# Performance work log

Measured on AMD Instinct MI355X. Metric: run time of the kernel, lower is better.

## Reference

```python
import jax, jax.numpy as jnp
import numpy as np

B, L, D = 4, 2048, 512   # batch, seq_len, model_dim
H, A = 8, 64             # head_num, atten_dim (H*A == D)
EPS = 1e-5


def setup_inputs() -> dict:
    key = jax.random.key(0)
    ks = jax.random.split(key, 20)
    std = 1.0 / np.sqrt(D)
    inp = {}
    for i, name in enumerate(["Q_data", "Q_time", "K_data", "K_time", "V_time"]):
        inp[name] = jax.random.normal(ks[i], (B, L, D), dtype=jnp.float32)
    # projection params (torch Linear: y = x @ W.T + b); store as [in, out]
    for i, name in enumerate(["Wq_d", "Wq_t", "Wk_d", "Wk_t", "Wv_t", "Wo"]):
        inp[name + "_w"] = jax.random.uniform(ks[5 + i], (D, H * A), jnp.float32, -std, std)
        inp[name + "_b"] = jax.random.uniform(ks[11 + i], (H * A,), jnp.float32, -std, std)
    inp["ln_g"] = jnp.ones((D,), jnp.float32)
    inp["ln_b"] = jnp.zeros((D,), jnp.float32)
    return inp


def _proj(x, w, b):
    # [B,L,D] -> [B,H,L,A]
    y = jnp.einsum('bld,de->ble', x, w) + b
    return y.reshape(B, L, H, A).transpose(0, 2, 1, 3)


def reference(Q_data, Q_time, K_data, K_time, V_time,
              Wq_d_w, Wq_t_w, Wk_d_w, Wk_t_w, Wv_t_w, Wo_w,
              Wq_d_b, Wq_t_b, Wk_d_b, Wk_t_b, Wv_t_b, Wo_b,
              ln_g, ln_b):
    residual = Q_data
    qd = _proj(Q_data, Wq_d_w, Wq_d_b)
    qt = _proj(Q_time, Wq_t_w, Wq_t_b)
    kd = _proj(K_data, Wk_d_w, Wk_d_b)
    kt = _proj(K_time, Wk_t_w, Wk_t_b)
    vt = _proj(V_time, Wv_t_w, Wv_t_b)
    scale = 1.0 / np.sqrt(A)
    # dual QK^T scores summed before softmax
    scores = (jnp.einsum('bhqa,bhka->bhqk', qd, kd)
              + jnp.einsum('bhqa,bhka->bhqk', qt, kt)) * scale
    attn = jax.nn.softmax(scores, axis=-1)
    ctx = jnp.einsum('bhqk,bhka->bhqa', attn, vt)        # [B,H,L,A]
    ctx = ctx.transpose(0, 2, 1, 3).reshape(B, L, H * A)  # [B,L,D]
    out = jnp.einsum('bld,de->ble', ctx, Wo_w) + Wo_b
    x = out + residual
    mu = jnp.mean(x, axis=-1, keepdims=True)
    var = jnp.var(x, axis=-1, keepdims=True)
    return (x - mu) / jnp.sqrt(var + EPS) * ln_g + ln_b
```

## Files before the change

kernel.cpp:

```cpp
#include <hip/hip_runtime.h>
#include <hip/hip_bf16.h>
#include <stdint.h>


using f32x4  = __attribute__((ext_vector_type(4))) float;
using bf16x8 = __attribute__((ext_vector_type(8))) short;

typedef __attribute__((address_space(1))) const uint32_t g_u32;
typedef __attribute__((address_space(3))) uint32_t l_u32;

#if __has_builtin(__builtin_amdgcn_exp2f)
#define EXP2F __builtin_amdgcn_exp2f
#else
#define EXP2F exp2f
#endif
#define QSCALE 0.1803368801111204f

__device__ __forceinline__ void glds16(const void* g, void* l) {
  __builtin_amdgcn_global_load_lds((g_u32*)g, (l_u32*)l, 16, 0, 0);
}

__device__ __forceinline__ unsigned short f2bfu(float f) {
  __hip_bfloat16 h = __float2bfloat16(f);
  union { __hip_bfloat16 h; unsigned short u; } v;
  v.h = h;
  return v.u;
}

__device__ __forceinline__ uint32_t pack_trunc(float lo, float hi) {
  union { float f; uint32_t u; } a, b;
  a.f = lo; b.f = hi;
  return __builtin_amdgcn_perm(b.u, a.u, 0x07060302u);
}

__global__ __launch_bounds__(256) void k_prep_w(
    const float* __restrict__ w0, const float* __restrict__ w1,
    const float* __restrict__ w2, const float* __restrict__ w3,
    const float* __restrict__ w4, const float* __restrict__ w5,
    unsigned short* __restrict__ wt) {
  __shared__ float tile[64][68];
  const float* wsrc[6] = {w0, w1, w2, w3, w4, w5};
  int bid = blockIdx.x;
  int mat = bid >> 6, tid = bid & 63;
  int k0 = (tid >> 3) << 6, c0 = (tid & 7) << 6;
  const float* w = wsrc[mat];
  int t = threadIdx.x;
  {
    int r = t >> 2, cq = (t & 3) << 4;
    const float4* src = reinterpret_cast<const float4*>(w + (size_t)(k0 + r) * 512 + c0 + cq);
#pragma unroll
    for (int j = 0; j < 4; ++j) {
      float4 v = src[j];
      tile[r][cq + j * 4 + 0] = v.x;
      tile[r][cq + j * 4 + 1] = v.y;
      tile[r][cq + j * 4 + 2] = v.z;
      tile[r][cq + j * 4 + 3] = v.w;
    }
  }
  __syncthreads();
  {
    int cc = t >> 2, kq = (t & 3) << 4;
    union { unsigned short u[16]; uint4 v[2]; } p;
#pragma unroll
    for (int j = 0; j < 16; ++j) p.u[j] = f2bfu(tile[kq + j][cc]);
    unsigned short* dst = wt + (size_t)mat * 262144 + (size_t)(c0 + cc) * 512 + k0 + kq;
    *reinterpret_cast<uint4*>(dst)     = p.v[0];
    *reinterpret_cast<uint4*>(dst + 8) = p.v[1];
  }
}

__global__ __launch_bounds__(512) void k_proj2(
    const float* __restrict__ x0, const float* __restrict__ x1,
    const float* __restrict__ x2, const float* __restrict__ x3,
    const float* __restrict__ x4,
    const unsigned short* __restrict__ wt,
    const float* __restrict__ b0, const float* __restrict__ b1,
    const float* __restrict__ b2, const float* __restrict__ b3,
    const float* __restrict__ b4,
    unsigned short* __restrict__ qws, unsigned short* __restrict__ kws,
    unsigned short* __restrict__ vws) {
  __shared__ __align__(16) unsigned short plds[24576];
  int bid = blockIdx.x;
  int proj = bid >> 8, rem = bid & 255;
  int cb = rem >> 6, rb = rem & 63;
  const float* xs[5] = {x0, x1, x2, x3, x4};
  const float* Ag = xs[proj] + (size_t)rb * 128 * 512;
  const unsigned short* Wg = wt + (size_t)proj * 262144 + (size_t)cb * 128 * 512;
  int t = threadIdx.x;
  int lane = t & 63, w = t >> 6, wr = w >> 2, wc = w & 3, g = lane >> 4, c = lane & 15;
  f32x4 acc[4][2];
#pragma unroll
  for (int i = 0; i < 4; ++i)
#pragma unroll
    for (int j = 0; j < 2; ++j) acc[i][j] = f32x4{0.f, 0.f, 0.f, 0.f};

  int srow[2], sch[2];
#pragma unroll
  for (int j = 0; j < 2; ++j) {
    int q = t + j * 512;
    srow[j] = q >> 3;
    sch[j] = q & 7;
  }
  float4 pa[2], pb[2];
#pragma unroll
  for (int j = 0; j < 2; ++j) {
    const float* src = Ag + (size_t)srow[j] * 512 + sch[j] * 8;
    pa[j] = *reinterpret_cast<const float4*>(src);
    pb[j] = *reinterpret_cast<const float4*>(src + 4);
  }
#pragma unroll
  for (int j = 0; j < 2; ++j) {
    int cid = t + j * 512;
    int row = cid >> 3, ch = cid & 7;
    glds16(Wg + (size_t)row * 512 + ((ch ^ (row & 7)) << 3),
           plds + 8192 + cid * 8);
  }

#pragma unroll 1
  for (int it = 0; it < 8; ++it) {
    int cur = it & 1;
    unsigned short* Bcur = plds + 8192 + cur * 8192;
    unsigned short* Bnxt = plds + 8192 + (cur ^ 1) * 8192;
    __syncthreads();
#pragma unroll
    for (int j = 0; j < 2; ++j) {
      union { unsigned short u[8]; uint4 v; } p;
      p.u[0] = f2bfu(pa[j].x); p.u[1] = f2bfu(pa[j].y);
      p.u[2] = f2bfu(pa[j].z); p.u[3] = f2bfu(pa[j].w);
      p.u[4] = f2bfu(pb[j].x); p.u[5] = f2bfu(pb[j].y);
      p.u[6] = f2bfu(pb[j].z); p.u[7] = f2bfu(pb[j].w);
      *reinterpret_cast<uint4*>(&plds[srow[j] * 64 + ((sch[j] ^ (srow[j] & 7)) << 3)]) = p.v;
    }
    __syncthreads();
    if (it < 7) {
#pragma unroll
      for (int j = 0; j < 2; ++j) {
        const float* src = Ag + (size_t)srow[j] * 512 + (it + 1) * 64 + sch[j] * 8;
        pa[j] = *reinterpret_cast<const float4*>(src);
        pb[j] = *reinterpret_cast<const float4*>(src + 4);
      }
#pragma unroll
      for (int j = 0; j < 2; ++j) {
        int cid = t + j * 512;
        int row = cid >> 3, ch = cid & 7;
        glds16(Wg + (size_t)row * 512 + (it + 1) * 64 + ((ch ^ (row & 7)) << 3),
               Bnxt + cid * 8);
      }
    }
#pragma unroll
    for (int fi = 0; fi < 2; ++fi) {
      bf16x8 af[4], bfr[2];
#pragma unroll
      for (int mi = 0; mi < 4; ++mi) {
        int arow = wr * 64 + mi * 16 + c;
        af[mi] = *reinterpret_cast<const bf16x8*>(
            &plds[arow * 64 + (((fi * 4 + g) ^ (arow & 7)) << 3)]);
      }
#pragma unroll
      for (int ni = 0; ni < 2; ++ni) {
        int brow = wc * 32 + ni * 16 + c;
        bfr[ni] = *reinterpret_cast<const bf16x8*>(
            &Bcur[brow * 64 + (((fi * 4 + g) ^ (brow & 7)) << 3)]);
      }
      __builtin_amdgcn_s_setprio(1);
#pragma unroll
      for (int mi = 0; mi < 4; ++mi)
#pragma unroll
        for (int ni = 0; ni < 2; ++ni)
          acc[mi][ni] = __builtin_amdgcn_mfma_f32_16x16x32_bf16(af[mi], bfr[ni], acc[mi][ni], 0, 0, 0);
      __builtin_amdgcn_s_setprio(0);
    }
  }

  const float* bias_arr[5] = {b0, b1, b2, b3, b4};
  const float* bias = bias_arr[proj];
  float scale = (proj < 2) ? QSCALE : 1.0f;
  int bglob = rb >> 4;
  int lbase = (rb & 15) * 128;
  __syncthreads();
  if (proj < 4) {
    unsigned short* qkdst = (proj < 2) ? qws : kws;
    int half = (proj & 1) ? 64 : 0;
#pragma unroll
    for (int ni = 0; ni < 2; ++ni) {
      int col = wc * 32 + ni * 16 + c;
      int colch = col >> 3, cw = col & 7;
      float bv = bias[cb * 128 + col];
#pragma unroll
      for (int mi = 0; mi < 4; ++mi)
#pragma unroll
        for (int rr = 0; rr < 4; ++rr) {
          int l_loc = wr * 64 + mi * 16 + g * 4 + rr;
          float v = (acc[mi][ni][rr] + bv) * scale;
          plds[l_loc * 128 + ((colch ^ (l_loc & 15)) << 3) + cw] = f2bfu(v);
        }
    }
    __syncthreads();
#pragma unroll
    for (int j = 0; j < 4; ++j) {
      int q = t + j * 512;
      int l_loc = q >> 4, ch = q & 15;
      uint4 d = *reinterpret_cast<const uint4*>(
          &plds[l_loc * 128 + ((ch ^ (l_loc & 15)) << 3)]);
      int n0 = cb * 128 + ch * 8;
      int h = n0 >> 6, a0 = n0 & 63;
      *reinterpret_cast<uint4*>(
          &qkdst[((size_t)(bglob * 8 + h) * 2048 + lbase + l_loc) * 128 + half + a0]) = d;
    }
  } else {
#pragma unroll
    for (int ni = 0; ni < 2; ++ni) {
      int n_loc = wc * 32 + ni * 16 + c;
      float bv = bias[cb * 128 + n_loc];
#pragma unroll
      for (int mi = 0; mi < 4; ++mi) {
        int P = ((mi & 2) << 4) | (g << 3) | ((mi & 1) << 2);
        int lp = wr * 64 + P;
        int c16 = lp >> 3, h8 = (lp >> 2) & 1;
        uint2 pk;
        pk.x = (uint32_t)f2bfu(acc[mi][ni][0] + bv) |
               ((uint32_t)f2bfu(acc[mi][ni][1] + bv) << 16);
        pk.y = (uint32_t)f2bfu(acc[mi][ni][2] + bv) |
               ((uint32_t)f2bfu(acc[mi][ni][3] + bv) << 16);
        *reinterpret_cast<uint2*>(
            &plds[(n_loc * 16 + (c16 ^ (n_loc & 15))) * 8 + h8 * 4]) = pk;
      }
    }
    __syncthreads();
#pragma unroll
    for (int j = 0; j < 4; ++j) {
      int q = t + j * 512;
      int n_loc = q & 127, c16 = q >> 7;
      uint4 d = *reinterpret_cast<const uint4*>(
          &plds[(n_loc * 16 + (c16 ^ (n_loc & 15))) * 8]);
      int n0 = cb * 128 + n_loc;
      int h = n0 >> 6, a = n0 & 63;
      *reinterpret_cast<uint4*>(
          &vws[((size_t)(bglob * 8 + h) * 64 + a) * 2048 + lbase + c16 * 8]) = d;
    }
  }
}

__device__ __forceinline__ void gemm_core(
    const unsigned short* Ag, const unsigned short* Wg,
    unsigned short* Al, unsigned short* Bl, f32x4 acc[4]) {
  int t = threadIdx.x;
  int lane = t & 63, w = t >> 6, g = lane >> 4, c = lane & 15;
#pragma unroll 1
  for (int it = 0; it < 8; ++it) {
    __syncthreads();
#pragma unroll
    for (int j = 0; j < 2; ++j) {
      int cid = t + j * 256;
      int row = cid >> 3, ch = cid & 7;
      glds16(Ag + (size_t)row * 512 + it * 64 + ((ch ^ (row & 7)) << 3), Al + cid * 8);
      glds16(Wg + (size_t)row * 512 + it * 64 + ((ch ^ (row & 7)) << 3), Bl + cid * 8);
    }
    __syncthreads();
#pragma unroll
    for (int fi = 0; fi < 2; ++fi) {
      int arow = w * 16 + c;
      bf16x8 af = *reinterpret_cast<const bf16x8*>(
          Al + arow * 64 + (((fi * 4 + g) ^ (arow & 7)) << 3));
#pragma unroll
      for (int ct = 0; ct < 4; ++ct) {
        int brow = ct * 16 + c;
        bf16x8 bf = *reinterpret_cast<const bf16x8*>(
            Bl + brow * 64 + (((fi * 4 + g) ^ (brow & 7)) << 3));
        acc[ct] = __builtin_amdgcn_mfma_f32_16x16x32_bf16(af, bf, acc[ct], 0, 0, 0);
      }
    }
  }
}

__global__ __launch_bounds__(256) void k_attn(
    const unsigned short* __restrict__ qws, const unsigned short* __restrict__ kws,
    const unsigned short* __restrict__ vws, unsigned short* __restrict__ ctxb) {
  __shared__ __align__(16) unsigned short alds[24576];
  int orig = blockIdx.x;
  int xcd = orig & 7, j = orig >> 3;
  int bh = xcd * 4 + (j >> 4), qb = j & 15;
  int t = threadIdx.x;
  int w = t >> 6, lane = t & 63, g = lane >> 4, c = lane & 15;

  const unsigned short* Kg = kws + (size_t)bh * 2048 * 128;
  const unsigned short* Vg = vws + (size_t)bh * 64 * 2048;

  bf16x8 qf[2][4];
#pragma unroll
  for (int qt = 0; qt < 2; ++qt) {
    const unsigned short* Qg =
        qws + ((size_t)bh * 2048 + qb * 128 + w * 32 + qt * 16 + c) * 128;
#pragma unroll
    for (int fi = 0; fi < 4; ++fi)
      qf[qt][fi] = *reinterpret_cast<const bf16x8*>(Qg + fi * 32 + g * 8);
  }

  f32x4 o[2][4];
#pragma unroll
  for (int qt = 0; qt < 2; ++qt)
#pragma unroll
    for (int at = 0; at < 4; ++at) o[qt][at] = f32x4{0.f, 0.f, 0.f, 0.f};
  float lsum[2] = {0.f, 0.f};

#pragma unroll
  for (int jj = 0; jj < 4; ++jj) {
    int cid = t + jj * 256;
    int row = cid >> 4, ch = cid & 15;
    glds16(Kg + (size_t)row * 128 + ((ch ^ (row & 15)) << 3), alds + cid * 8);
  }
#pragma unroll
  for (int jj = 0; jj < 2; ++jj) {
    int cid = t + jj * 256;
    int a = cid >> 3, ch = cid & 7;
    glds16(Vg + (size_t)a * 2048 + ((ch ^ (a & 7)) << 3), alds + 16384 + cid * 8);
  }
  __syncthreads();

#pragma unroll 1
  for (int it = 0; it < 32; ++it) {
    int cur = it & 1;
    unsigned short* Kcur = alds + cur * 8192;
    unsigned short* Vcur = alds + 16384 + cur * 4096;
    if (it < 31) {
      unsigned short* Knxt = alds + (cur ^ 1) * 8192;
      unsigned short* Vnxt = alds + 16384 + (cur ^ 1) * 4096;
#pragma unroll
      for (int jj = 0; jj < 4; ++jj) {
        int cid = t + jj * 256;
        int row = cid >> 4, ch = cid & 15;
        glds16(Kg + ((size_t)(it + 1) * 64 + row) * 128 + ((ch ^ (row & 15)) << 3),
               Knxt + cid * 8);
      }
#pragma unroll
      for (int jj = 0; jj < 2; ++jj) {
        int cid = t + jj * 256;
        int a = cid >> 3, ch = cid & 7;
        glds16(Vg + (size_t)a * 2048 + (it + 1) * 64 + ((ch ^ (a & 7)) << 3),
               Vnxt + cid * 8);
      }
    }

    f32x4 s[2][4];
#pragma unroll
    for (int qt = 0; qt < 2; ++qt)
#pragma unroll
      for (int mt = 0; mt < 4; ++mt) s[qt][mt] = f32x4{0.f, 0.f, 0.f, 0.f};
#pragma unroll
    for (int fi = 0; fi < 4; ++fi) {
      bf16x8 kf[4];
#pragma unroll
      for (int mt = 0; mt < 4; ++mt)
        kf[mt] = *reinterpret_cast<const bf16x8*>(
            &Kcur[(mt * 16 + c) * 128 + (((fi * 4 + g) ^ c) << 3)]);
      __builtin_amdgcn_s_setprio(1);
#pragma unroll
      for (int mt = 0; mt < 4; ++mt) {
        s[0][mt] = __builtin_amdgcn_mfma_f32_16x16x32_bf16(kf[mt], qf[0][fi], s[0][mt], 0, 0, 0);
        s[1][mt] = __builtin_amdgcn_mfma_f32_16x16x32_bf16(kf[mt], qf[1][fi], s[1][mt], 0, 0, 0);
      }
      __builtin_amdgcn_s_setprio(0);
    }

    uint32_t pku[2][4][2];
#pragma unroll
    for (int qt = 0; qt < 2; ++qt) {
      float ls = 0.f;
#pragma unroll
      for (int mt = 0; mt < 4; ++mt) {
        float p0 = EXP2F(s[qt][mt][0]);
        float p1 = EXP2F(s[qt][mt][1]);
        float p2 = EXP2F(s[qt][mt][2]);
        float p3 = EXP2F(s[qt][mt][3]);
        ls += (p0 + p1) + (p2 + p3);
        pku[qt][mt][0] = pack_trunc(p0, p1);
        pku[qt][mt][1] = pack_trunc(p2, p3);
      }
      lsum[qt] += ls;
    }

    union u32x4_bf { uint32_t u[4]; bf16x8 v; };
    u32x4_bf pf[2][2];
#pragma unroll
    for (int qt = 0; qt < 2; ++qt) {
      pf[qt][0].u[0] = pku[qt][0][0]; pf[qt][0].u[1] = pku[qt][0][1];
      pf[qt][0].u[2] = pku[qt][1][0]; pf[qt][0].u[3] = pku[qt][1][1];
      pf[qt][1].u[0] = pku[qt][2][0]; pf[qt][1].u[1] = pku[qt][2][1];
      pf[qt][1].u[2] = pku[qt][3][0]; pf[qt][1].u[3] = pku[qt][3][1];
    }
#pragma unroll
    for (int at = 0; at < 4; ++at) {
      int arow = at * 16 + c;
      bf16x8 vf0 = *reinterpret_cast<const bf16x8*>(
          &Vcur[arow * 64 + ((g ^ (arow & 7)) << 3)]);
      bf16x8 vf1 = *reinterpret_cast<const bf16x8*>(
          &Vcur[arow * 64 + (((4 + g) ^ (arow & 7)) << 3)]);
      __builtin_amdgcn_s_setprio(1);
#pragma unroll
      for (int qt = 0; qt < 2; ++qt) {
        o[qt][at] = __builtin_amdgcn_mfma_f32_16x16x32_bf16(pf[qt][0].v, vf0, o[qt][at], 0, 0, 0);
        o[qt][at] = __builtin_amdgcn_mfma_f32_16x16x32_bf16(pf[qt][1].v, vf1, o[qt][at], 0, 0, 0);
      }
      __builtin_amdgcn_s_setprio(0);
    }
    __syncthreads();
  }

  int b = bh >> 3, h = bh & 7;
#pragma unroll
  for (int qt = 0; qt < 2; ++qt) {
    lsum[qt] += __shfl_xor(lsum[qt], 16);
    lsum[qt] += __shfl_xor(lsum[qt], 32);
    float rinv[4];
#pragma unroll
    for (int r = 0; r < 4; ++r) rinv[r] = 1.0f / __shfl(lsum[qt], g * 4 + r);
#pragma unroll
    for (int at = 0; at < 4; ++at) {
      int col = at * 16 + c;
      int colch = col >> 3, cw = col & 7;
#pragma unroll
      for (int r = 0; r < 4; ++r) {
        int l_loc = w * 32 + qt * 16 + g * 4 + r;
        alds[l_loc * 64 + ((colch ^ (l_loc & 7)) << 3) + cw] = f2bfu(o[qt][at][r] * rinv[r]);
      }
    }
  }
  __syncthreads();
#pragma unroll
  for (int jj = 0; jj < 4; ++jj) {
    int q = t + jj * 256;
    int l_loc = q >> 3, ch = q & 7;
    uint4 d = *reinterpret_cast<const uint4*>(
        &alds[l_loc * 64 + ((ch ^ (l_loc & 7)) << 3)]);
    *reinterpret_cast<uint4*>(
        &ctxb[(size_t)(b * 2048 + qb * 128 + l_loc) * 512 + h * 64 + ch * 8]) = d;
  }
}

__global__ __launch_bounds__(256) void k_oproj(
    const unsigned short* __restrict__ ctxb, const unsigned short* __restrict__ wt,
    const float* __restrict__ bo, const float* __restrict__ resid,
    float* __restrict__ out) {
  __shared__ __align__(16) unsigned short oplds[8192];
  int bid = blockIdx.x;
  int rb = bid >> 3, cb = bid & 7;
  const unsigned short* Ag = ctxb + (size_t)rb * 64 * 512;
  const unsigned short* Wg = wt + (size_t)5 * 262144 + (size_t)cb * 64 * 512;
  f32x4 acc[4];
#pragma unroll
  for (int i = 0; i < 4; ++i) acc[i] = f32x4{0.f, 0.f, 0.f, 0.f};
  gemm_core(Ag, Wg, oplds, oplds + 4096, acc);
  int t = threadIdx.x;
  int lane = t & 63, w = t >> 6, g = lane >> 4, c = lane & 15;
  __syncthreads();
  float* fl = reinterpret_cast<float*>(oplds);
#pragma unroll
  for (int ct = 0; ct < 4; ++ct) {
    int col = ct * 16 + c;
    int colch = col >> 2, cw = col & 3;
    float bv = bo[cb * 64 + col];
#pragma unroll
    for (int r = 0; r < 4; ++r) {
      int l_loc = w * 16 + g * 4 + r;
      fl[l_loc * 64 + ((colch ^ (l_loc & 15)) << 2) + cw] = acc[ct][r] + bv;
    }
  }
  __syncthreads();
#pragma unroll
  for (int j = 0; j < 4; ++j) {
    int q = t + j * 256;
    int l_loc = q >> 4, ch = q & 15;
    f32x4 d = *reinterpret_cast<const f32x4*>(
        &fl[l_loc * 64 + ((ch ^ (l_loc & 15)) << 2)]);
    size_t di = (size_t)(rb * 64 + l_loc) * 512 + cb * 64 + ch * 4;
    f32x4 rs = *reinterpret_cast<const f32x4*>(&resid[di]);
    *reinterpret_cast<f32x4*>(&out[di]) = d + rs;
  }
}

__global__ __launch_bounds__(256) void k_ln(float* __restrict__ out,
                                            const float* __restrict__ gam,
                                            const float* __restrict__ bet) {
  int row = blockIdx.x * 4 + (threadIdx.x >> 6);
  int lane = threadIdx.x & 63;
  float* x = out + (size_t)row * 512 + lane * 8;
  float4 v0 = reinterpret_cast<const float4*>(x)[0];
  float4 v1 = reinterpret_cast<const float4*>(x)[1];
  float s = v0.x + v0.y + v0.z + v0.w + v1.x + v1.y + v1.z + v1.w;
  float q = v0.x * v0.x + v0.y * v0.y + v0.z * v0.z + v0.w * v0.w +
            v1.x * v1.x + v1.y * v1.y + v1.z * v1.z + v1.w * v1.w;
#pragma unroll
  for (int d = 1; d < 64; d <<= 1) {
    s += __shfl_xor(s, d);
    q += __shfl_xor(q, d);
  }
  float mu = s * (1.0f / 512.0f);
  float var = q * (1.0f / 512.0f) - mu * mu;
  float rstd = rsqrtf(var + 1e-5f);
  float4 g0 = reinterpret_cast<const float4*>(gam + lane * 8)[0];
  float4 g1 = reinterpret_cast<const float4*>(gam + lane * 8)[1];
  float4 b0 = reinterpret_cast<const float4*>(bet + lane * 8)[0];
  float4 b1 = reinterpret_cast<const float4*>(bet + lane * 8)[1];
  v0.x = (v0.x - mu) * rstd * g0.x + b0.x;
  v0.y = (v0.y - mu) * rstd * g0.y + b0.y;
  v0.z = (v0.z - mu) * rstd * g0.z + b0.z;
  v0.w = (v0.w - mu) * rstd * g0.w + b0.w;
  v1.x = (v1.x - mu) * rstd * g1.x + b1.x;
  v1.y = (v1.y - mu) * rstd * g1.y + b1.y;
  v1.z = (v1.z - mu) * rstd * g1.z + b1.z;
  v1.w = (v1.w - mu) * rstd * g1.w + b1.w;
  reinterpret_cast<float4*>(x)[0] = v0;
  reinterpret_cast<float4*>(x)[1] = v1;
}

extern "C" void kernel_launch(void* const* d_in, const int* in_sizes, int n_in,
                              void* d_out, int out_size, void* d_ws, size_t ws_size,
                              hipStream_t stream) {
  const float* Qd  = (const float*)d_in[0];
  const float* Qt  = (const float*)d_in[1];
  const float* Kd  = (const float*)d_in[2];
  const float* Kt  = (const float*)d_in[3];
  const float* Vt  = (const float*)d_in[4];
  const float* Wqd = (const float*)d_in[5];
  const float* bqd = (const float*)d_in[6];
  const float* Wqt = (const float*)d_in[7];
  const float* bqt = (const float*)d_in[8];
  const float* Wkd = (const float*)d_in[9];
  const float* bkd = (const float*)d_in[10];
  const float* Wkt = (const float*)d_in[11];
  const float* bkt = (const float*)d_in[12];
  const float* Wvt = (const float*)d_in[13];
  const float* bvt = (const float*)d_in[14];
  const float* Wo  = (const float*)d_in[15];
  const float* bo  = (const float*)d_in[16];
  const float* lng = (const float*)d_in[17];
  const float* lnb = (const float*)d_in[18];

  char* ws = (char*)d_ws;
  unsigned short* wt   = (unsigned short*)(ws);
  unsigned short* qws  = (unsigned short*)(ws + 3145728);
  unsigned short* kws  = (unsigned short*)(ws + 19922944);
  unsigned short* vws  = (unsigned short*)(ws + 36700160);
  unsigned short* ctxb = (unsigned short*)(ws + 45088768);
  float* out = (float*)d_out;

  k_prep_w<<<384, 256, 0, stream>>>(Wqd, Wqt, Wkd, Wkt, Wvt, Wo, wt);
  k_proj2<<<1280, 512, 0, stream>>>(Qd, Qt, Kd, Kt, Vt, wt,
                                    bqd, bqt, bkd, bkt, bvt, qws, kws, vws);
  k_attn<<<512, 256, 0, stream>>>(qws, kws, vws, ctxb);
  k_oproj<<<1024, 256, 0, stream>>>(ctxb, wt, bo, Qd, out);
  k_ln<<<2048, 256, 0, stream>>>(out, lng, lnb);
}
```

Baseline: 127.2 us.

## Fuse output projection with residual add and LayerNorm in one kernel

```diff
diff --git a/kernel.cpp b/kernel.cpp
--- a/kernel.cpp
+++ b/kernel.cpp
@@ -241,38 +241,6 @@
   }
 }
 
-__device__ __forceinline__ void gemm_core(
-    const unsigned short* Ag, const unsigned short* Wg,
-    unsigned short* Al, unsigned short* Bl, f32x4 acc[4]) {
-  int t = threadIdx.x;
-  int lane = t & 63, w = t >> 6, g = lane >> 4, c = lane & 15;
-#pragma unroll 1
-  for (int it = 0; it < 8; ++it) {
-    __syncthreads();
-#pragma unroll
-    for (int j = 0; j < 2; ++j) {
-      int cid = t + j * 256;
-      int row = cid >> 3, ch = cid & 7;
-      glds16(Ag + (size_t)row * 512 + it * 64 + ((ch ^ (row & 7)) << 3), Al + cid * 8);
-      glds16(Wg + (size_t)row * 512 + it * 64 + ((ch ^ (row & 7)) << 3), Bl + cid * 8);
-    }
-    __syncthreads();
-#pragma unroll
-    for (int fi = 0; fi < 2; ++fi) {
-      int arow = w * 16 + c;
-      bf16x8 af = *reinterpret_cast<const bf16x8*>(
-          Al + arow * 64 + (((fi * 4 + g) ^ (arow & 7)) << 3));
-#pragma unroll
-      for (int ct = 0; ct < 4; ++ct) {
-        int brow = ct * 16 + c;
-        bf16x8 bf = *reinterpret_cast<const bf16x8*>(
-            Bl + brow * 64 + (((fi * 4 + g) ^ (brow & 7)) << 3));
-        acc[ct] = __builtin_amdgcn_mfma_f32_16x16x32_bf16(af, bf, acc[ct], 0, 0, 0);
-      }
-    }
-  }
-}
-
 __global__ __launch_bounds__(256) void k_attn(
     const unsigned short* __restrict__ qws, const unsigned short* __restrict__ kws,
     const unsigned short* __restrict__ vws, unsigned short* __restrict__ ctxb) {
@@ -437,80 +405,119 @@
   }
 }
 
-__global__ __launch_bounds__(256) void k_oproj(
+__global__ __launch_bounds__(512) void k_oproj_ln(
     const unsigned short* __restrict__ ctxb, const unsigned short* __restrict__ wt,
     const float* __restrict__ bo, const float* __restrict__ resid,
+    const float* __restrict__ gam, const float* __restrict__ bet,
     float* __restrict__ out) {
-  __shared__ __align__(16) unsigned short oplds[8192];
-  int bid = blockIdx.x;
-  int rb = bid >> 3, cb = bid & 7;
+  __shared__ __align__(16) unsigned short olds[36864];
+  int rb = blockIdx.x;
   const unsigned short* Ag = ctxb + (size_t)rb * 64 * 512;
-  const unsigned short* Wg = wt + (size_t)5 * 262144 + (size_t)cb * 64 * 512;
-  f32x4 acc[4];
-#pragma unroll
-  for (int i = 0; i < 4; ++i) acc[i] = f32x4{0.f, 0.f, 0.f, 0.f};
-  gemm_core(Ag, Wg, oplds, oplds + 4096, acc);
+  const unsigned short* Wg = wt + (size_t)5 * 262144;
   int t = threadIdx.x;
   int lane = t & 63, w = t >> 6, g = lane >> 4, c = lane & 15;
-  __syncthreads();
-  float* fl = reinterpret_cast<float*>(oplds);
-#pragma unroll
-  for (int ct = 0; ct < 4; ++ct) {
-    int col = ct * 16 + c;
-    int colch = col >> 2, cw = col & 3;
-    float bv = bo[cb * 64 + col];
-#pragma unroll
-    for (int r = 0; r < 4; ++r) {
-      int l_loc = w * 16 + g * 4 + r;
-      fl[l_loc * 64 + ((colch ^ (l_loc & 15)) << 2) + cw] = acc[ct][r] + bv;
-    }
-  }
-  __syncthreads();
-#pragma unroll
-  for (int j = 0; j < 4; ++j) {
-    int q = t + j * 256;
-    int l_loc = q >> 4, ch = q & 15;
-    f32x4 d = *reinterpret_cast<const f32x4*>(
-        &fl[l_loc * 64 + ((ch ^ (l_loc & 15)) << 2)]);
-    size_t di = (size_t)(rb * 64 + l_loc) * 512 + cb * 64 + ch * 4;
-    f32x4 rs = *reinterpret_cast<const f32x4*>(&resid[di]);
-    *reinterpret_cast<f32x4*>(&out[di]) = d + rs;
-  }
-}
-
-__global__ __launch_bounds__(256) void k_ln(float* __restrict__ out,
-                                            const float* __restrict__ gam,
-                                            const float* __restrict__ bet) {
-  int row = blockIdx.x * 4 + (threadIdx.x >> 6);
-  int lane = threadIdx.x & 63;
-  float* x = out + (size_t)row * 512 + lane * 8;
-  float4 v0 = reinterpret_cast<const float4*>(x)[0];
-  float4 v1 = reinterpret_cast<const float4*>(x)[1];
-  float s = v0.x + v0.y + v0.z + v0.w + v1.x + v1.y + v1.z + v1.w;
-  float q = v0.x * v0.x + v0.y * v0.y + v0.z * v0.z + v0.w * v0.w +
-            v1.x * v1.x + v1.y * v1.y + v1.z * v1.z + v1.w * v1.w;
-#pragma unroll
-  for (int d = 1; d < 64; d <<= 1) {
-    s += __shfl_xor(s, d);
-    q += __shfl_xor(q, d);
-  }
-  float mu = s * (1.0f / 512.0f);
-  float var = q * (1.0f / 512.0f) - mu * mu;
-  float rstd = rsqrtf(var + 1e-5f);
-  float4 g0 = reinterpret_cast<const float4*>(gam + lane * 8)[0];
-  float4 g1 = reinterpret_cast<const float4*>(gam + lane * 8)[1];
-  float4 b0 = reinterpret_cast<const float4*>(bet + lane * 8)[0];
-  float4 b1 = reinterpret_cast<const float4*>(bet + lane * 8)[1];
-  v0.x = (v0.x - mu) * rstd * g0.x + b0.x;
-  v0.y = (v0.y - mu) * rstd * g0.y + b0.y;
-  v0.z = (v0.z - mu) * rstd * g0.z + b0.z;
-  v0.w = (v0.w - mu) * rstd * g0.w + b0.w;
-  v1.x = (v1.x - mu) * rstd * g1.x + b1.x;
-  v1.y = (v1.y - mu) * rstd * g1.y + b1.y;
-  v1.z = (v1.z - mu) * rstd * g1.z + b1.z;
-  v1.w = (v1.w - mu) * rstd * g1.w + b1.w;
-  reinterpret_cast<float4*>(x)[0] = v0;
-  reinterpret_cast<float4*>(x)[1] = v1;
+  unsigned short* Bl = olds;
+  unsigned short* Al = olds + 32768;
+  f32x4 acc[4][4];
+#pragma unroll
+  for (int i = 0; i < 4; ++i)
+#pragma unroll
+    for (int j = 0; j < 4; ++j) acc[i][j] = f32x4{0.f, 0.f, 0.f, 0.f};
+
+#pragma unroll 1
+  for (int it = 0; it < 8; ++it) {
+    __syncthreads();
+    {
+      int row = t >> 3, ch = t & 7;
+      glds16(Ag + (size_t)row * 512 + it * 64 + ((ch ^ (row & 7)) << 3), Al + t * 8);
+    }
+#pragma unroll
+    for (int j = 0; j < 8; ++j) {
+      int cid = t + j * 512;
+      int row = cid >> 3, ch = cid & 7;
+      glds16(Wg + (size_t)row * 512 + it * 64 + ((ch ^ (row & 7)) << 3), Bl + cid * 8);
+    }
+    __syncthreads();
+#pragma unroll
+    for (int fi = 0; fi < 2; ++fi) {
+      bf16x8 af[4], bfr[4];
+#pragma unroll
+      for (int mi = 0; mi < 4; ++mi) {
+        int arow = mi * 16 + c;
+        af[mi] = *reinterpret_cast<const bf16x8*>(
+            &Al[arow * 64 + (((fi * 4 + g) ^ (arow & 7)) << 3)]);
+      }
+#pragma unroll
+      for (int ni = 0; ni < 4; ++ni) {
+        int brow = w * 64 + ni * 16 + c;
+        bfr[ni] = *reinterpret_cast<const bf16x8*>(
+            &Bl[brow * 64 + (((fi * 4 + g) ^ (brow & 7)) << 3)]);
+      }
+      __builtin_amdgcn_s_setprio(1);
+#pragma unroll
+      for (int mi = 0; mi < 4; ++mi)
+#pragma unroll
+        for (int ni = 0; ni < 4; ++ni)
+          acc[mi][ni] = __builtin_amdgcn_mfma_f32_16x16x32_bf16(af[mi], bfr[ni], acc[mi][ni], 0, 0, 0);
+      __builtin_amdgcn_s_setprio(0);
+    }
+  }
+
+  float* fl = reinterpret_cast<float*>(olds);
+  int erow = t >> 4;
+  int ei = t & 15;
+#pragma unroll 1
+  for (int h = 0; h < 2; ++h) {
+    __syncthreads();
+#pragma unroll
+    for (int mi2 = 0; mi2 < 2; ++mi2) {
+      int mi = h * 2 + mi2;
+#pragma unroll
+      for (int ni = 0; ni < 4; ++ni) {
+        int col = w * 64 + ni * 16 + c;
+        int colch = col >> 2, cw = col & 3;
+        float bv = bo[col];
+#pragma unroll
+        for (int r = 0; r < 4; ++r) {
+          int l_loc = mi2 * 16 + g * 4 + r;
+          fl[l_loc * 512 + ((colch ^ (l_loc & 7)) << 2) + cw] = acc[mi][ni][r] + bv;
+        }
+      }
+    }
+    __syncthreads();
+    int rowg = rb * 64 + h * 32 + erow;
+    f32x4 xv[8];
+    float sum = 0.f, ssq = 0.f;
+#pragma unroll
+    for (int k = 0; k < 8; ++k) {
+      int ci = ei * 8 + ((k + ei) & 7);
+      f32x4 v = *reinterpret_cast<const f32x4*>(
+          &fl[erow * 512 + (((ci) ^ (erow & 7)) << 2)]);
+      f32x4 rs = *reinterpret_cast<const f32x4*>(&resid[(size_t)rowg * 512 + ci * 4]);
+      v = v + rs;
+      xv[k] = v;
+      sum += v[0] + v[1] + v[2] + v[3];
+      ssq += v[0] * v[0] + v[1] * v[1] + v[2] * v[2] + v[3] * v[3];
+    }
+#pragma unroll
+    for (int d = 1; d < 16; d <<= 1) {
+      sum += __shfl_xor(sum, d);
+      ssq += __shfl_xor(ssq, d);
+    }
+    float mu = sum * (1.0f / 512.0f);
+    float var = ssq * (1.0f / 512.0f) - mu * mu;
+    float rstd = rsqrtf(var + 1e-5f);
+#pragma unroll
+    for (int k = 0; k < 8; ++k) {
+      int ci = ei * 8 + ((k + ei) & 7);
+      f32x4 gm = *reinterpret_cast<const f32x4*>(&gam[ci * 4]);
+      f32x4 bt = *reinterpret_cast<const f32x4*>(&bet[ci * 4]);
+      f32x4 v = xv[k];
+#pragma unroll
+      for (int e = 0; e < 4; ++e) v[e] = (v[e] - mu) * rstd * gm[e] + bt[e];
+      *reinterpret_cast<f32x4*>(&out[(size_t)rowg * 512 + ci * 4]) = v;
+    }
+  }
 }
 
 extern "C" void kernel_launch(void* const* d_in, const int* in_sizes, int n_in,
@@ -548,6 +555,5 @@
   k_proj2<<<1280, 512, 0, stream>>>(Qd, Qt, Kd, Kt, Vt, wt,
                                     bqd, bqt, bkd, bkt, bvt, qws, kws, vws);
   k_attn<<<512, 256, 0, stream>>>(qws, kws, vws, ctxb);
-  k_oproj<<<1024, 256, 0, stream>>>(ctxb, wt, bo, Qd, out);
-  k_ln<<<2048, 256, 0, stream>>>(out, lng, lnb);
-}
+  k_oproj_ln<<<128, 512, 0, stream>>>(ctxb, wt, bo, Qd, lng, lnb, out);
+}
```

After: 161.5 us. +27.0%, slower.
